# Optimization experiments

Hardware: AMD Instinct MI355X
Metric: run time of the kernel (lower is better)

The kernel has to match this reference:

```python
import jax, jax.numpy as jnp
import numpy as np

N_HEAD = 16

def setup_inputs() -> dict:
    key = jax.random.key(0)
    ks = jax.random.split(key, 5)
    B, T, C = 4, 2048, 1024
    x = jax.random.normal(ks[0], (B, T, C), dtype=jnp.float32)
    # Linear params (torch nn.Linear: y = x @ W.T + b), init scaled like default
    s = 1.0 / np.sqrt(C)
    W_attn = jax.random.uniform(ks[1], (3 * C, C), dtype=jnp.float32, minval=-s, maxval=s)
    b_attn = jax.random.uniform(ks[2], (3 * C,), dtype=jnp.float32, minval=-s, maxval=s)
    W_proj = jax.random.uniform(ks[3], (C, C), dtype=jnp.float32, minval=-s, maxval=s)
    b_proj = jax.random.uniform(ks[4], (C,), dtype=jnp.float32, minval=-s, maxval=s)
    return {"x": x, "W_attn": W_attn, "b_attn": b_attn, "W_proj": W_proj, "b_proj": b_proj}

def reference(x, W_attn, b_attn, W_proj, b_proj):
    B, T, C = x.shape
    H = N_HEAD
    D = C // H
    qkv = jnp.einsum('btc,oc->bto', x, W_attn) + b_attn  # [B,T,3C]
    q, k, v = jnp.split(qkv, 3, axis=2)
    # [B,H,T,D]
    q = q.reshape(B, T, H, D).transpose(0, 2, 1, 3)
    k = k.reshape(B, T, H, D).transpose(0, 2, 1, 3)
    v = v.reshape(B, T, H, D).transpose(0, 2, 1, 3)
    att = jnp.einsum('bhtd,bhsd->bhts', q, k) * (1.0 / np.sqrt(D))  # [B,H,T,T]
    causal = jnp.tril(jnp.ones((T, T), dtype=bool))
    att = jnp.where(causal, att, -jnp.inf)
    att = jax.nn.softmax(att, axis=-1)
    y = jnp.einsum('bhts,bhsd->bhtd', att, v)  # [B,H,T,D]
    y = y.transpose(0, 2, 1, 3).reshape(B, T, C)
    return jnp.einsum('btc,oc->bto', y, W_proj) + b_proj
```

## Files before the change

kernel.cpp:

```cpp
#include <hip/hip_runtime.h>
#include <stdint.h>

typedef unsigned short u16;
typedef __attribute__((ext_vector_type(8))) short short8;
typedef __attribute__((ext_vector_type(4))) float float4v;

#define MFMA16(a, b, c) __builtin_amdgcn_mfma_f32_16x16x32_bf16((a), (b), (c), 0, 0, 0)

#define Q_SCALE 0.18033688011112042f

__device__ __forceinline__ int swz(int row, int col) {
  return row * 64 + (col & 7) + ((((col >> 3) ^ row) & 7) << 3);
}

__device__ __forceinline__ u16 f2b(float f) {
  union { float f; unsigned u; } x; x.f = f;
  unsigned r = x.u + 0x7fffu + ((x.u >> 16) & 1u);
  return (u16)(r >> 16);
}

__device__ __forceinline__ unsigned pack2(float a, float b) {
  return (unsigned)f2b(a) | ((unsigned)f2b(b) << 16);
}

__device__ __forceinline__ void load_lds_16(const void* g, void* l) {
  __builtin_amdgcn_global_load_lds((__attribute__((address_space(1))) void*)g,
                                   (__attribute__((address_space(3))) void*)l,
                                   16, 0, 0);
}

__global__ __launch_bounds__(256) void cvt_bf16(const float* __restrict__ in,
                                                u16* __restrict__ out, int n8) {
  int i = blockIdx.x * 256 + threadIdx.x;
  if (i >= n8) return;
  const float4* p = (const float4*)in + (size_t)i * 2;
  float4 a = p[0], b = p[1];
  uint4 w;
  w.x = pack2(a.x, a.y);
  w.y = pack2(a.z, a.w);
  w.z = pack2(b.x, b.y);
  w.w = pack2(b.z, b.w);
  *(uint4*)&out[(size_t)i * 8] = w;
}

__global__ __launch_bounds__(256) void transpose_v(const u16* __restrict__ V,
                                                   u16* __restrict__ Vt) {
  __shared__ u16 tile[64][72];
  const int bh = blockIdx.y;
  const int t0 = blockIdx.x * 64;
  const int tid = threadIdx.x;
  const int r = tid >> 3, c = (tid & 7) * 8;
#pragma unroll
  for (int h = 0; h < 2; ++h) {
    uint4 v = *(const uint4*)&V[((size_t)bh * 2048 + t0 + r + h * 32) * 64 + c];
    const u16* p = (const u16*)&v;
#pragma unroll
    for (int j = 0; j < 8; ++j) tile[c + j][r + h * 32] = p[j];
  }
  __syncthreads();
#pragma unroll
  for (int h = 0; h < 2; ++h) {
    uint4 w;
    u16* p = (u16*)&w;
#pragma unroll
    for (int j = 0; j < 8; ++j) p[j] = tile[r + h * 32][c + j];
    *(uint4*)&Vt[((size_t)bh * 64 + r + h * 32) * 2048 + t0 + c] = w;
  }
}

template <bool QKV_OUT>
__global__ __launch_bounds__(256) void gemm_bt(const u16* __restrict__ A,
                                               const u16* __restrict__ B,
                                               const float* __restrict__ bias,
                                               float* __restrict__ Cf,
                                               u16* __restrict__ QKV,
                                               int M, int N, int K) {
  __shared__ __align__(16) u16 As[128 * 64];
  __shared__ __align__(16) u16 Bs[128 * 64];
  const int tid = threadIdx.x;
  const int lane = tid & 63;
  const int wave = tid >> 6;
  const int quad = lane >> 4;
  const int l15 = lane & 15;
  const int bm0 = blockIdx.y * 128;
  const int bn0 = blockIdx.x * 128;
  const int wm = (wave & 1) * 64;
  const int wn = (wave >> 1) * 64;

  float4v acc[4][4];
#pragma unroll
  for (int i = 0; i < 4; ++i)
#pragma unroll
    for (int j = 0; j < 4; ++j) acc[i][j] = (float4v){0.f, 0.f, 0.f, 0.f};

  const int srow = wave * 32 + (lane >> 3);
  const int scol = ((lane & 7) ^ ((lane >> 3) & 7)) * 8;

  for (int k0 = 0; k0 < K; k0 += 64) {
#pragma unroll
    for (int s = 0; s < 4; ++s) {
      const int r = s * 8;
      load_lds_16(&A[(size_t)(bm0 + srow + r) * K + k0 + scol], &As[(wave * 32 + r) * 64]);
      load_lds_16(&B[(size_t)(bn0 + srow + r) * K + k0 + scol], &Bs[(wave * 32 + r) * 64]);
    }
    __builtin_amdgcn_s_waitcnt(0);
    __syncthreads();
#pragma unroll
    for (int ks = 0; ks < 2; ++ks) {
      short8 af[4], bf[4];
#pragma unroll
      for (int t = 0; t < 4; ++t) {
        af[t] = *(const short8*)&As[swz(wm + t * 16 + l15, ks * 32 + quad * 8)];
        bf[t] = *(const short8*)&Bs[swz(wn + t * 16 + l15, ks * 32 + quad * 8)];
      }
#pragma unroll
      for (int mt = 0; mt < 4; ++mt)
#pragma unroll
        for (int nt = 0; nt < 4; ++nt)
          acc[mt][nt] = MFMA16(af[mt], bf[nt], acc[mt][nt]);
    }
    __syncthreads();
  }

#pragma unroll
  for (int mt = 0; mt < 4; ++mt) {
    const int row0 = bm0 + wm + mt * 16 + quad * 4;
#pragma unroll
    for (int nt = 0; nt < 4; ++nt) {
      const int col = bn0 + wn + nt * 16 + l15;
      const float bs = bias[col];
      if constexpr (QKV_OUT) {
        const int which = col >> 10;
        const int rem = col & 1023;
        const int h = rem >> 6;
        const int d = rem & 63;
        const float sc = (which == 0) ? Q_SCALE : 1.0f;
#pragma unroll
        for (int i = 0; i < 4; ++i) {
          const int t = row0 + i;
          const int b = t >> 11;
          const int tt = t & 2047;
          QKV[(size_t)which * 8388608 +
              ((size_t)(b * 16 + h) * 2048 + tt) * 64 + d] = f2b((acc[mt][nt][i] + bs) * sc);
        }
      } else {
#pragma unroll
        for (int i = 0; i < 4; ++i)
          Cf[(size_t)(row0 + i) * N + col] = acc[mt][nt][i] + bs;
      }
    }
  }
}

__global__ __launch_bounds__(256) void attn_kernel(const u16* __restrict__ QKV,
                                                   const u16* __restrict__ Vt_g,
                                                   u16* __restrict__ Y) {
  const int bx = blockIdx.x;
  const int bh = blockIdx.y;
  const int b = bh >> 4, h = bh & 15;
  const int tid = threadIdx.x;
  const int lane = tid & 63;
  const int wave = tid >> 6;
  const int quad = lane >> 4;
  const int l15 = lane & 15;

  const u16* Qg = QKV + (size_t)bh * 2048 * 64;
  const u16* Kg = QKV + 8388608 + (size_t)bh * 2048 * 64;
  const u16* Vg = Vt_g + (size_t)bh * 64 * 2048;

  __shared__ __align__(16) u16 Ks[2][64 * 64];
  __shared__ __align__(16) u16 Vt[2][64 * 64];

  short8 qf[2];
#pragma unroll
  for (int ks = 0; ks < 2; ++ks)
    qf[ks] = *(const short8*)&Qg[(size_t)(bx * 64 + wave * 16 + l15) * 64 + ks * 32 + quad * 8];

  float4v o[4];
  float rs = 0.f;
#pragma unroll
  for (int i = 0; i < 4; ++i) o[i] = (float4v){0.f, 0.f, 0.f, 0.f};

  const int idxA = (l15 + ((quad & 1) << 5)) << 2;
  const int idxB = idxA + 64;

  const int r8 = lane >> 3;
  const int c8 = ((lane & 7) ^ r8) * 8;
  auto stage = [&](int st_, int bufi) {
    const int sb = st_ * 64;
#pragma unroll
    for (int p = 0; p < 2; ++p) {
      const int c = wave * 2 + p;
      load_lds_16(&Kg[(size_t)(sb + c * 8 + r8) * 64 + c8], &Ks[bufi][c * 512]);
      load_lds_16(&Vg[(size_t)(c * 8 + r8) * 2048 + sb + c8], &Vt[bufi][c * 512]);
    }
  };

  stage(0, 0);
  __builtin_amdgcn_s_waitcnt(0);
  __syncthreads();

  for (int st = 0; st <= bx; ++st) {
    const int cur = st & 1;
    if (st < bx) stage(st + 1, cur ^ 1);

    float4v s[4];
#pragma unroll
    for (int nt = 0; nt < 4; ++nt) s[nt] = (float4v){0.f, 0.f, 0.f, 0.f};
    __builtin_amdgcn_s_setprio(1);
#pragma unroll
    for (int ks = 0; ks < 2; ++ks)
#pragma unroll
      for (int nt = 0; nt < 4; ++nt) {
        const short8 kf = *(const short8*)&Ks[cur][swz(nt * 16 + l15, ks * 32 + quad * 8)];
        s[nt] = MFMA16(kf, qf[ks], s[nt]);
      }
    __builtin_amdgcn_s_setprio(0);

    if (st == bx) {
      const int qrow = wave * 16 + l15;
      const int kb = quad * 4;
#pragma unroll
      for (int nt = 0; nt < 4; ++nt)
#pragma unroll
        for (int i = 0; i < 4; ++i)
          if (kb + nt * 16 + i > qrow) s[nt][i] = -1e30f;
    }

    uint2 pk[4];
#pragma unroll
    for (int nt = 0; nt < 4; ++nt) {
      const float p0 = __builtin_amdgcn_exp2f(s[nt][0]);
      const float p1 = __builtin_amdgcn_exp2f(s[nt][1]);
      const float p2 = __builtin_amdgcn_exp2f(s[nt][2]);
      const float p3 = __builtin_amdgcn_exp2f(s[nt][3]);
      rs += (p0 + p1) + (p2 + p3);
      pk[nt].x = pack2(p0, p1);
      pk[nt].y = pack2(p2, p3);
    }

    short8 af[2];
    const bool hi = quad >= 2;
#pragma unroll
    for (int ks = 0; ks < 2; ++ks) {
      const int a0 = __builtin_amdgcn_ds_bpermute(idxA, (int)pk[2 * ks].x);
      const int a1 = __builtin_amdgcn_ds_bpermute(idxA, (int)pk[2 * ks].y);
      const int b0 = __builtin_amdgcn_ds_bpermute(idxA, (int)pk[2 * ks + 1].x);
      const int b1 = __builtin_amdgcn_ds_bpermute(idxA, (int)pk[2 * ks + 1].y);
      const int c0 = __builtin_amdgcn_ds_bpermute(idxB, (int)pk[2 * ks].x);
      const int c1 = __builtin_amdgcn_ds_bpermute(idxB, (int)pk[2 * ks].y);
      const int d0 = __builtin_amdgcn_ds_bpermute(idxB, (int)pk[2 * ks + 1].x);
      const int d1 = __builtin_amdgcn_ds_bpermute(idxB, (int)pk[2 * ks + 1].y);
      uint4 w;
      w.x = (unsigned)(hi ? b0 : a0);
      w.y = (unsigned)(hi ? b1 : a1);
      w.z = (unsigned)(hi ? d0 : c0);
      w.w = (unsigned)(hi ? d1 : c1);
      af[ks] = *(const short8*)&w;
    }

    __builtin_amdgcn_s_setprio(1);
#pragma unroll
    for (int ks = 0; ks < 2; ++ks)
#pragma unroll
      for (int dt = 0; dt < 4; ++dt) {
        const short8 vf = *(const short8*)&Vt[cur][swz(dt * 16 + l15, ks * 32 + quad * 8)];
        o[dt] = MFMA16(af[ks], vf, o[dt]);
      }
    __builtin_amdgcn_s_setprio(0);

    __builtin_amdgcn_s_waitcnt(0);
    __syncthreads();
  }

  float r = rs;
  r += __shfl_xor(r, 16);
  r += __shfl_xor(r, 32);
  float linv[4];
#pragma unroll
  for (int i = 0; i < 4; ++i) linv[i] = 1.0f / __shfl(r, quad * 4 + i);
#pragma unroll
  for (int dt = 0; dt < 4; ++dt)
#pragma unroll
    for (int i = 0; i < 4; ++i) {
      const float v = o[dt][i] * linv[i];
      const int t = bx * 64 + wave * 16 + quad * 4 + i;
      Y[((size_t)b * 2048 + t) * 1024 + h * 64 + dt * 16 + l15] = f2b(v);
    }
}

extern "C" void kernel_launch(void* const* d_in, const int* in_sizes, int n_in,
                              void* d_out, int out_size, void* d_ws, size_t ws_size,
                              hipStream_t stream) {
  const float* x  = (const float*)d_in[0];
  const float* Wa = (const float*)d_in[1];
  const float* ba = (const float*)d_in[2];
  const float* Wp = (const float*)d_in[3];
  const float* bp = (const float*)d_in[4];
  float* out = (float*)d_out;

  u16* xb  = (u16*)d_ws;
  u16* Wab = xb + 8388608;
  u16* Wpb = Wab + 3145728;
  u16* qkv = Wpb + 1048576;
  u16* y   = xb;
  u16* vt  = (u16*)d_out;

  cvt_bf16<<<4096, 256, 0, stream>>>(x, xb, 1048576);
  cvt_bf16<<<1536, 256, 0, stream>>>(Wa, Wab, 393216);
  cvt_bf16<<<512, 256, 0, stream>>>(Wp, Wpb, 131072);

  gemm_bt<true><<<dim3(24, 64), 256, 0, stream>>>(xb, Wab, ba, nullptr, qkv, 8192, 3072, 1024);
  transpose_v<<<dim3(32, 64), 256, 0, stream>>>(qkv + 16777216, vt);
  attn_kernel<<<dim3(32, 64), 256, 0, stream>>>(qkv, vt, y);
  gemm_bt<false><<<dim3(8, 64), 256, 0, stream>>>(y, Wpb, bp, out, nullptr, 8192, 1024, 1024);
}
```

Baseline: 320.7 us.

## Pair causal query tiles per block to balance attention work and share K/V loads

Each attention block now handles two query tiles, bx and 31-bx, so every block does the same number of key/value steps. The K/V tiles staged in LDS are reused by both query tiles where both need them, which halves K/V traffic for the shared range and removes the tail imbalance of the causal triangle. The cost is a grid of half as many blocks (1024), doubled accumulator registers, which may lower occupancy, and a data-dependent branch inside the loop.

```diff
diff --git a/kernel.cpp b/kernel.cpp
--- a/kernel.cpp
+++ b/kernel.cpp
@@ -163,6 +163,7 @@
   const int wave = tid >> 6;
   const int quad = lane >> 4;
   const int l15 = lane & 15;
+  const int qt[2] = {bx, 31 - bx};
 
   const u16* Qg = QKV + (size_t)bh * 2048 * 64;
   const u16* Kg = QKV + 8388608 + (size_t)bh * 2048 * 64;
@@ -171,15 +172,19 @@
   __shared__ __align__(16) u16 Ks[2][64 * 64];
   __shared__ __align__(16) u16 Vt[2][64 * 64];
 
-  short8 qf[2];
-#pragma unroll
-  for (int ks = 0; ks < 2; ++ks)
-    qf[ks] = *(const short8*)&Qg[(size_t)(bx * 64 + wave * 16 + l15) * 64 + ks * 32 + quad * 8];
-
-  float4v o[4];
-  float rs = 0.f;
-#pragma unroll
-  for (int i = 0; i < 4; ++i) o[i] = (float4v){0.f, 0.f, 0.f, 0.f};
+  short8 qf[2][2];
+#pragma unroll
+  for (int u = 0; u < 2; ++u)
+#pragma unroll
+    for (int ks = 0; ks < 2; ++ks)
+      qf[u][ks] = *(const short8*)&Qg[(size_t)(qt[u] * 64 + wave * 16 + l15) * 64 + ks * 32 + quad * 8];
+
+  float4v o[2][4];
+  float rs[2] = {0.f, 0.f};
+#pragma unroll
+  for (int u = 0; u < 2; ++u)
+#pragma unroll
+    for (int i = 0; i < 4; ++i) o[u][i] = (float4v){0.f, 0.f, 0.f, 0.f};
 
   const int idxA = (l15 + ((quad & 1) << 5)) << 2;
   const int idxB = idxA + 64;
@@ -196,67 +201,77 @@
     }
   };
 
+  const int last = qt[1];
   stage(0, 0);
   __builtin_amdgcn_s_waitcnt(0);
   __syncthreads();
 
-  for (int st = 0; st <= bx; ++st) {
+  for (int st = 0; st <= last; ++st) {
     const int cur = st & 1;
-    if (st < bx) stage(st + 1, cur ^ 1);
-
-    float4v s[4];
-#pragma unroll
-    for (int nt = 0; nt < 4; ++nt) s[nt] = (float4v){0.f, 0.f, 0.f, 0.f};
+    if (st < last) stage(st + 1, cur ^ 1);
+    const bool both = (st <= qt[0]);
+
+    float4v s[2][4];
+#pragma unroll
+    for (int u = 0; u < 2; ++u)
+#pragma unroll
+      for (int nt = 0; nt < 4; ++nt) s[u][nt] = (float4v){0.f, 0.f, 0.f, 0.f};
     __builtin_amdgcn_s_setprio(1);
 #pragma unroll
     for (int ks = 0; ks < 2; ++ks)
 #pragma unroll
       for (int nt = 0; nt < 4; ++nt) {
         const short8 kf = *(const short8*)&Ks[cur][swz(nt * 16 + l15, ks * 32 + quad * 8)];
-        s[nt] = MFMA16(kf, qf[ks], s[nt]);
+        s[1][nt] = MFMA16(kf, qf[1][ks], s[1][nt]);
+        if (both) s[0][nt] = MFMA16(kf, qf[0][ks], s[0][nt]);
       }
     __builtin_amdgcn_s_setprio(0);
 
-    if (st == bx) {
-      const int qrow = wave * 16 + l15;
-      const int kb = quad * 4;
-#pragma unroll
-      for (int nt = 0; nt < 4; ++nt)
-#pragma unroll
-        for (int i = 0; i < 4; ++i)
-          if (kb + nt * 16 + i > qrow) s[nt][i] = -1e30f;
-    }
-
-    uint2 pk[4];
-#pragma unroll
-    for (int nt = 0; nt < 4; ++nt) {
-      const float p0 = __builtin_amdgcn_exp2f(s[nt][0]);
-      const float p1 = __builtin_amdgcn_exp2f(s[nt][1]);
-      const float p2 = __builtin_amdgcn_exp2f(s[nt][2]);
-      const float p3 = __builtin_amdgcn_exp2f(s[nt][3]);
-      rs += (p0 + p1) + (p2 + p3);
-      pk[nt].x = pack2(p0, p1);
-      pk[nt].y = pack2(p2, p3);
-    }
-
-    short8 af[2];
+    short8 af[2][2];
     const bool hi = quad >= 2;
 #pragma unroll
-    for (int ks = 0; ks < 2; ++ks) {
-      const int a0 = __builtin_amdgcn_ds_bpermute(idxA, (int)pk[2 * ks].x);
-      const int a1 = __builtin_amdgcn_ds_bpermute(idxA, (int)pk[2 * ks].y);
-      const int b0 = __builtin_amdgcn_ds_bpermute(idxA, (int)pk[2 * ks + 1].x);
-      const int b1 = __builtin_amdgcn_ds_bpermute(idxA, (int)pk[2 * ks + 1].y);
-      const int c0 = __builtin_amdgcn_ds_bpermute(idxB, (int)pk[2 * ks].x);
-      const int c1 = __builtin_amdgcn_ds_bpermute(idxB, (int)pk[2 * ks].y);
-      const int d0 = __builtin_amdgcn_ds_bpermute(idxB, (int)pk[2 * ks + 1].x);
-      const int d1 = __builtin_amdgcn_ds_bpermute(idxB, (int)pk[2 * ks + 1].y);
-      uint4 w;
-      w.x = (unsigned)(hi ? b0 : a0);
-      w.y = (unsigned)(hi ? b1 : a1);
-      w.z = (unsigned)(hi ? d0 : c0);
-      w.w = (unsigned)(hi ? d1 : c1);
-      af[ks] = *(const short8*)&w;
+    for (int u = 0; u < 2; ++u) {
+      if (u == 0 && !both) continue;
+
+      if (st == qt[u]) {
+        const int qrow = wave * 16 + l15;
+        const int kb = quad * 4;
+#pragma unroll
+        for (int nt = 0; nt < 4; ++nt)
+#pragma unroll
+          for (int i = 0; i < 4; ++i)
+            if (kb + nt * 16 + i > qrow) s[u][nt][i] = -1e30f;
+      }
+
+      uint2 pk[4];
+#pragma unroll
+      for (int nt = 0; nt < 4; ++nt) {
+        const float p0 = __builtin_amdgcn_exp2f(s[u][nt][0]);
+        const float p1 = __builtin_amdgcn_exp2f(s[u][nt][1]);
+        const float p2 = __builtin_amdgcn_exp2f(s[u][nt][2]);
+        const float p3 = __builtin_amdgcn_exp2f(s[u][nt][3]);
+        rs[u] += (p0 + p1) + (p2 + p3);
+        pk[nt].x = pack2(p0, p1);
+        pk[nt].y = pack2(p2, p3);
+      }
+
+#pragma unroll
+      for (int ks = 0; ks < 2; ++ks) {
+        const int a0 = __builtin_amdgcn_ds_bpermute(idxA, (int)pk[2 * ks].x);
+        const int a1 = __builtin_amdgcn_ds_bpermute(idxA, (int)pk[2 * ks].y);
+        const int b0 = __builtin_amdgcn_ds_bpermute(idxA, (int)pk[2 * ks + 1].x);
+        const int b1 = __builtin_amdgcn_ds_bpermute(idxA, (int)pk[2 * ks + 1].y);
+        const int c0 = __builtin_amdgcn_ds_bpermute(idxB, (int)pk[2 * ks].x);
+        const int c1 = __builtin_amdgcn_ds_bpermute(idxB, (int)pk[2 * ks].y);
+        const int d0 = __builtin_amdgcn_ds_bpermute(idxB, (int)pk[2 * ks + 1].x);
+        const int d1 = __builtin_amdgcn_ds_bpermute(idxB, (int)pk[2 * ks + 1].y);
+        uint4 w;
+        w.x = (unsigned)(hi ? b0 : a0);
+        w.y = (unsigned)(hi ? b1 : a1);
+        w.z = (unsigned)(hi ? d0 : c0);
+        w.w = (unsigned)(hi ? d1 : c1);
+        af[u][ks] = *(const short8*)&w;
+      }
     }
 
     __builtin_amdgcn_s_setprio(1);
@@ -265,7 +280,8 @@
 #pragma unroll
       for (int dt = 0; dt < 4; ++dt) {
         const short8 vf = *(const short8*)&Vt[cur][swz(dt * 16 + l15, ks * 32 + quad * 8)];
-        o[dt] = MFMA16(af[ks], vf, o[dt]);
+        o[1][dt] = MFMA16(af[1][ks], vf, o[1][dt]);
+        if (both) o[0][dt] = MFMA16(af[0][ks], vf, o[0][dt]);
       }
     __builtin_amdgcn_s_setprio(0);
 
@@ -273,20 +289,23 @@
     __syncthreads();
   }
 
-  float r = rs;
-  r += __shfl_xor(r, 16);
-  r += __shfl_xor(r, 32);
-  float linv[4];
-#pragma unroll
-  for (int i = 0; i < 4; ++i) linv[i] = 1.0f / __shfl(r, quad * 4 + i);
-#pragma unroll
-  for (int dt = 0; dt < 4; ++dt)
-#pragma unroll
-    for (int i = 0; i < 4; ++i) {
-      const float v = o[dt][i] * linv[i];
-      const int t = bx * 64 + wave * 16 + quad * 4 + i;
-      Y[((size_t)b * 2048 + t) * 1024 + h * 64 + dt * 16 + l15] = f2b(v);
-    }
+#pragma unroll
+  for (int u = 0; u < 2; ++u) {
+    float r = rs[u];
+    r += __shfl_xor(r, 16);
+    r += __shfl_xor(r, 32);
+    float linv[4];
+#pragma unroll
+    for (int i = 0; i < 4; ++i) linv[i] = 1.0f / __shfl(r, quad * 4 + i);
+#pragma unroll
+    for (int dt = 0; dt < 4; ++dt)
+#pragma unroll
+      for (int i = 0; i < 4; ++i) {
+        const float v = o[u][dt][i] * linv[i];
+        const int t = qt[u] * 64 + wave * 16 + quad * 4 + i;
+        Y[((size_t)b * 2048 + t) * 1024 + h * 64 + dt * 16 + l15] = f2b(v);
+      }
+  }
 }
 
 extern "C" void kernel_launch(void* const* d_in, const int* in_sizes, int n_in,
@@ -312,6 +331,6 @@
 
   gemm_bt<true><<<dim3(24, 64), 256, 0, stream>>>(xb, Wab, ba, nullptr, qkv, 8192, 3072, 1024);
   transpose_v<<<dim3(32, 64), 256, 0, stream>>>(qkv + 16777216, vt);
-  attn_kernel<<<dim3(32, 64), 256, 0, stream>>>(qkv, vt, y);
+  attn_kernel<<<dim3(16, 64), 256, 0, stream>>>(qkv, vt, y);
   gemm_bt<false><<<dim3(8, 64), 256, 0, stream>>>(y, Wpb, bp, out, nullptr, 8192, 1024, 1024);
 }
```

After: 315.7 us. About the same (-1.6%).
